# Kernel optimization log

Measured on AMD Instinct MI355X. Metric: run time of the kernel, lower is better.

Reference implementation:

```python
import jax, jax.numpy as jnp
import numpy as np

THRESHOLD = 0.9
EPS = 1e-12


def setup_inputs() -> dict:
    key = jax.random.key(0)
    ks = jax.random.split(key, 7)
    B, D_in, H1, H2, D_out = 8192, 256, 512, 256, 64
    # torch Linear default init ~ U(-1/sqrt(fan_in), 1/sqrt(fan_in)); randn scaled is fine as a stand-in
    def lin(k, out_f, in_f):
        return jax.random.normal(k, (out_f, in_f), dtype=jnp.float32) / np.sqrt(in_f)
    return {
        "x": jax.random.normal(ks[0], (B, D_in), dtype=jnp.float32),
        "W1": lin(ks[1], H1, D_in),
        "b1": jax.random.normal(ks[2], (H1,), dtype=jnp.float32) * 0.01,
        "W2": lin(ks[3], H2, H1),
        "b2": jax.random.normal(ks[4], (H2,), dtype=jnp.float32) * 0.01,
        "W3": lin(ks[5], D_out, H2),
        "b3": jax.random.normal(ks[6], (D_out,), dtype=jnp.float32) * 0.01,
    }


def reference(x, W1, b1, W2, b2, W3, b3):
    # MLP: Linear -> Tanh -> Linear -> Tanh -> Linear (no tanh on last)
    h1 = jnp.tanh(x @ W1.T + b1)          # [B, 512]
    h2 = jnp.tanh(h1 @ W2.T + b2)         # [B, 256]
    out = h2 @ W3.T + b3                  # [B, 64]

    # Pairwise state fidelity: (normalized dot)^2, thresholded adjacency (diag excluded)
    norms = jnp.linalg.norm(out, axis=-1, keepdims=True)  # [B, 1]
    normed = out / (norms + EPS)
    fid = (normed @ normed.T) ** 2                         # [B, B]
    adj = (fid >= THRESHOLD).astype(out.dtype)
    B = out.shape[0]
    adj = adj * (1.0 - jnp.eye(B, dtype=out.dtype))        # no self-edges (i < j pairs only)

    return adj @ out                                       # [B, 64]
```

## Files before the change

kernel.cpp:

```cpp
#include <hip/hip_runtime.h>
#include <hip/hip_bf16.h>
#include <math.h>

#define B_ROWS 8192
#define D_IN   256
#define H1_DIM 512
#define H2_DIM 256
#define D_OUT  64
#define EPSF   1e-12f
#define THRESH 0.9f
#define BAND_LO 0.89f
#define BAND_HI 0.91f

typedef __attribute__((ext_vector_type(8))) short short8;
typedef __attribute__((ext_vector_type(4))) float f32x4;

__device__ inline void pack8(const float* __restrict__ src, short* __restrict__ dh,
                             short* __restrict__ dm, int t, int C, int lgq) {
  const int lane = t & 63;
  const int g = t >> 6;
  const int q = g & ((1 << lgq) - 1);
  const int I = g >> lgq;
  const int row = I * 16 + (lane & 15);
  const int k0 = q * 32 + ((lane >> 4) << 3);
  const float* p = src + (size_t)row * C + k0;
  float4 a = *(const float4*)p;
  float4 b = *(const float4*)(p + 4);
  float v[8] = {a.x, a.y, a.z, a.w, b.x, b.y, b.z, b.w};
  short h8[8], m8[8];
#pragma unroll
  for (int e = 0; e < 8; ++e) {
    __hip_bfloat16 h = __float2bfloat16(v[e]);
    float hf = __bfloat162float(h);
    __hip_bfloat16 m = __float2bfloat16(v[e] - hf);
    h8[e] = *(short*)&h;
    m8[e] = *(short*)&m;
  }
  *(short8*)(dh + (size_t)t * 8) = *(short8*)h8;
  *(short8*)(dm + (size_t)t * 8) = *(short8*)m8;
}

__global__ __launch_bounds__(256)
void pack_inputs(const float* __restrict__ x, const float* __restrict__ W1,
                 const float* __restrict__ W2, const float* __restrict__ W3,
                 short* xh, short* xm, short* w1h, short* w1m,
                 short* w2h, short* w2m, short* w3h, short* w3m) {
  const int b = blockIdx.x;
  const int tid = threadIdx.x;
  if (b < 1024)       pack8(x,  xh,  xm,  b * 256 + tid, 256, 3);
  else if (b < 1088)  pack8(W1, w1h, w1m, (b - 1024) * 256 + tid, 256, 3);
  else if (b < 1152)  pack8(W2, w2h, w2m, (b - 1088) * 256 + tid, 512, 4);
  else                pack8(W3, w3h, w3m, (b - 1152) * 256 + tid, 256, 3);
}

template<int KSTEPS, int JT, int MODE>
__global__ __launch_bounds__(256, 2)
void mfma_gemm(const short* __restrict__ pAh, const short* __restrict__ pAm,
               const short* __restrict__ pBh, const short* __restrict__ pBm,
               const float* __restrict__ bias, float* __restrict__ Cout,
               short* __restrict__ dh, short* __restrict__ dm, int N,
               float* __restrict__ rz) {
  constexpr int ITB = 4;
  constexpr int BTJ = 2 * JT;
  constexpr int NITEMS = 2 * ITB + 2 * BTJ;
  constexpr int PER_WAVE = NITEMS / 4;
  constexpr int WCOL = 16 * JT + 4;
  union SM {
    struct {
      short Ah[2][ITB * 512];
      short Am[2][ITB * 512];
      short Bh[2][BTJ * 512];
      short Bm[2][BTJ * 512];
    } st;
    float wbuf[4 * 32 * WCOL];
  };
  __shared__ __align__(16) SM sm;
  __shared__ float nsum[2][64];
  __shared__ float invn[64];

  const int tid = threadIdx.x;
  const int wave = tid >> 6, lane = tid & 63;
  const int wi = wave >> 1, wj = wave & 1;
  const int bIt0 = blockIdx.x * ITB;
  const int bJt0 = blockIdx.y * BTJ;

  if constexpr (MODE == 2) {
    float4* rz4 = (float4*)(rz + (size_t)blockIdx.x * 64 * 64);
#pragma unroll
    for (int u = 0; u < 4; ++u)
      rz4[u * 256 + tid] = make_float4(0.f, 0.f, 0.f, 0.f);
  }

  f32x4 acc[2][JT];
#pragma unroll
  for (int a = 0; a < 2; ++a)
#pragma unroll
    for (int b = 0; b < JT; ++b) acc[a][b] = (f32x4){0.f, 0.f, 0.f, 0.f};

  auto stage = [&](int q, int bf) {
#pragma unroll
    for (int u = 0; u < PER_WAVE; ++u) {
      const int item = wave * PER_WAVE + u;
      const short* src;
      short* dst;
      if (item < 2 * ITB) {
        const int t = item >> 1;
        const int m = item & 1;
        src = (m ? pAm : pAh) + ((size_t)(bIt0 + t) * KSTEPS + q) * 512;
        dst = (m ? sm.st.Am : sm.st.Ah)[bf] + t * 512;
      } else {
        const int e = item - 2 * ITB;
        const int t = e >> 1;
        const int m = e & 1;
        src = (m ? pBm : pBh) + ((size_t)(bJt0 + t) * KSTEPS + q) * 512;
        dst = (m ? sm.st.Bm : sm.st.Bh)[bf] + t * 512;
      }
      __builtin_amdgcn_global_load_lds(
          (const __attribute__((address_space(1))) void*)(src + lane * 8),
          (__attribute__((address_space(3))) void*)dst, 16, 0, 0);
    }
  };

  stage(0, 0);
  for (int q = 0; q < KSTEPS; ++q) {
    __syncthreads();
    if (q + 1 < KSTEPS) stage(q + 1, (q + 1) & 1);
    const int bf = q & 1;
    short8 Ah[2], Am[2];
#pragma unroll
    for (int it = 0; it < 2; ++it) {
      Ah[it] = *(const short8*)(sm.st.Ah[bf] + (wi * 2 + it) * 512 + lane * 8);
      Am[it] = *(const short8*)(sm.st.Am[bf] + (wi * 2 + it) * 512 + lane * 8);
    }
    short8 Bh[JT], Bm[JT];
#pragma unroll
    for (int jt = 0; jt < JT; ++jt) {
      Bh[jt] = *(const short8*)(sm.st.Bh[bf] + (wj * JT + jt) * 512 + lane * 8);
      Bm[jt] = *(const short8*)(sm.st.Bm[bf] + (wj * JT + jt) * 512 + lane * 8);
    }
#pragma unroll
    for (int it = 0; it < 2; ++it)
#pragma unroll
      for (int jt = 0; jt < JT; ++jt) {
        acc[it][jt] = __builtin_amdgcn_mfma_f32_16x16x32_bf16(Ah[it], Bh[jt], acc[it][jt], 0, 0, 0);
        acc[it][jt] = __builtin_amdgcn_mfma_f32_16x16x32_bf16(Ah[it], Bm[jt], acc[it][jt], 0, 0, 0);
        acc[it][jt] = __builtin_amdgcn_mfma_f32_16x16x32_bf16(Am[it], Bh[jt], acc[it][jt], 0, 0, 0);
      }
  }
  __syncthreads();

  float bv[JT];
#pragma unroll
  for (int jt = 0; jt < JT; ++jt)
    bv[jt] = bias[(bJt0 + wj * JT + jt) * 16 + (lane & 15)];

  if constexpr (MODE == 1) {
#pragma unroll
    for (int it = 0; it < 2; ++it)
#pragma unroll
      for (int jt = 0; jt < JT; ++jt)
#pragma unroll
        for (int r = 0; r < 4; ++r) {
          const float val = tanhf(acc[it][jt][r] + bv[jt]);
          const int row_l = it * 16 + (lane >> 4) * 4 + r;
          const int col_l = jt * 16 + (lane & 15);
          sm.wbuf[(wave * 32 + row_l) * WCOL + col_l] = val;
        }
    __syncthreads();
  } else {
#pragma unroll
    for (int it = 0; it < 2; ++it)
#pragma unroll
      for (int r = 0; r < 4; ++r) {
        float sq = 0.f;
        const int row_l = it * 16 + (lane >> 4) * 4 + r;
#pragma unroll
        for (int jt = 0; jt < JT; ++jt) {
          const float val = acc[it][jt][r] + bv[jt];
          const int col_l = jt * 16 + (lane & 15);
          sm.wbuf[(wave * 32 + row_l) * WCOL + col_l] = val;
          const int row = (bIt0 + wi * 2 + it) * 16 + (lane >> 4) * 4 + r;
          Cout[(size_t)row * N + wj * (16 * JT) + col_l] = val;
          sq = fmaf(val, val, sq);
        }
#pragma unroll
        for (int m = 1; m < 16; m <<= 1) sq += __shfl_xor(sq, m, 64);
        if ((lane & 15) == 0) nsum[wj][wi * 32 + row_l] = sq;
      }
    __syncthreads();
    if (tid < 64) invn[tid] = 1.0f / (sqrtf(nsum[0][tid] + nsum[1][tid]) + EPSF);
    __syncthreads();
  }

  constexpr int QLMAX = (JT >= 2) ? (JT / 2) : 1;
#pragma unroll
  for (int itl = 0; itl < 2; ++itl)
#pragma unroll
    for (int ql = 0; ql < QLMAX; ++ql) {
      const int row_l = itl * 16 + (lane & 15);
      const int kl = ql * 32 + ((lane >> 4) << 3);
      const float* wp = &sm.wbuf[(wave * 32 + row_l) * WCOL + kl];
      const float scale = (MODE == 2) ? invn[wi * 32 + row_l] : 1.0f;
      float4 a = *(const float4*)wp;
      float4 b = *(const float4*)(wp + 4);
      float v[8] = {a.x, a.y, a.z, a.w, b.x, b.y, b.z, b.w};
      short h8[8], m8[8];
#pragma unroll
      for (int e = 0; e < 8; ++e) {
        const float sv = v[e] * scale;
        __hip_bfloat16 h = __float2bfloat16(sv);
        float hf = __bfloat162float(h);
        __hip_bfloat16 m = __float2bfloat16(sv - hf);
        h8[e] = *(short*)&h;
        m8[e] = *(short*)&m;
      }
      const int ItG = bIt0 + wi * 2 + itl;
      const int qG = (((bJt0 + wj * JT) * 16) + ql * 32) >> 5;
      const size_t off = ((size_t)(ItG * (N >> 5) + qG) * 64 + lane) * 8;
      *(short8*)(dh + off) = *(short8*)h8;
      *(short8*)(dm + off) = *(short8*)m8;
    }
}

__global__ __launch_bounds__(256, 2)
void gram_accum(const short* __restrict__ vph, const short* __restrict__ vpm,
                const float* __restrict__ out, float* __restrict__ res) {
  __shared__ __align__(16) short lAh[8 * 1024];
  __shared__ __align__(16) short lAm[8 * 1024];
  const int tid = threadIdx.x;
  const int wave = tid >> 6, lane = tid & 63;

  const int t = blockIdx.x;
  int I = (int)((129.0f - sqrtf(16641.0f - 8.0f * (float)t)) * 0.5f);
  if (I < 0) I = 0;
  while (64 * (I + 1) - ((I + 1) * I) / 2 <= t) ++I;
  while (64 * I - (I * (I - 1)) / 2 > t) --I;
  const int Jc = I + (t - (64 * I - (I * (I - 1)) / 2));
  const int i0 = I * 128;
  const int j0c = Jc * 128;

  {
    const size_t base = (size_t)I * 8192;
#pragma unroll
    for (int u = 0; u < 8; ++u) {
      const int item = wave * 8 + u;
      const short* src;
      short* dst;
      if (item < 16) { src = vph + base + item * 512; dst = lAh + item * 512; }
      else           { src = vpm + base + (item - 16) * 512; dst = lAm + (item - 16) * 512; }
      __builtin_amdgcn_global_load_lds(
          (const __attribute__((address_space(1))) void*)(src + lane * 8),
          (__attribute__((address_space(3))) void*)dst, 16, 0, 0);
    }
  }
  __syncthreads();

  short8 Ah[8][2];
#pragma unroll
  for (int it = 0; it < 8; ++it)
#pragma unroll
    for (int q = 0; q < 2; ++q)
      Ah[it][q] = *(const short8*)(lAh + it * 1024 + q * 512 + lane * 8);

#pragma unroll
  for (int tt = 0; tt < 2; ++tt) {
    const int jt = wave * 2 + tt;
    const int j0 = j0c + jt * 16;
    const short* jb_h = vph + (size_t)(j0 >> 4) * 1024;
    short8 Bh0 = *(const short8*)(jb_h + lane * 8);
    short8 Bh1 = *(const short8*)(jb_h + 512 + lane * 8);

    f32x4 g[8];
#pragma unroll
    for (int it = 0; it < 8; ++it) g[it] = (f32x4){0.f, 0.f, 0.f, 0.f};
#pragma unroll
    for (int it = 0; it < 8; ++it) g[it] = __builtin_amdgcn_mfma_f32_16x16x32_bf16(Ah[it][0], Bh0, g[it], 0, 0, 0);
#pragma unroll
    for (int it = 0; it < 8; ++it) g[it] = __builtin_amdgcn_mfma_f32_16x16x32_bf16(Ah[it][1], Bh1, g[it], 0, 0, 0);

    bool band = false;
#pragma unroll
    for (int it = 0; it < 8; ++it)
#pragma unroll
      for (int r = 0; r < 4; ++r) {
        const float f = g[it][r] * g[it][r];
        band = band || (f > BAND_LO && f < BAND_HI);
      }
    if (__any(band)) {
      const short* jb_m = vpm + (size_t)(j0 >> 4) * 1024;
      short8 Bm0 = *(const short8*)(jb_m + lane * 8);
      short8 Bm1 = *(const short8*)(jb_m + 512 + lane * 8);
#pragma unroll
      for (int it = 0; it < 8; ++it) g[it] = __builtin_amdgcn_mfma_f32_16x16x32_bf16(Ah[it][0], Bm0, g[it], 0, 0, 0);
#pragma unroll
      for (int it = 0; it < 8; ++it) g[it] = __builtin_amdgcn_mfma_f32_16x16x32_bf16(Ah[it][1], Bm1, g[it], 0, 0, 0);
#pragma unroll
      for (int it = 0; it < 8; ++it) {
        short8 Am0 = *(const short8*)(lAm + it * 1024 + lane * 8);
        short8 Am1 = *(const short8*)(lAm + it * 1024 + 512 + lane * 8);
        g[it] = __builtin_amdgcn_mfma_f32_16x16x32_bf16(Am0, Bh0, g[it], 0, 0, 0);
        g[it] = __builtin_amdgcn_mfma_f32_16x16x32_bf16(Am1, Bh1, g[it], 0, 0, 0);
      }
    }

    const int j = j0 + (lane & 15);
#pragma unroll
    for (int it = 0; it < 8; ++it) {
      const float m01 = fmaxf(g[it][0] * g[it][0], g[it][1] * g[it][1]);
      const float m23 = fmaxf(g[it][2] * g[it][2], g[it][3] * g[it][3]);
      if (fmaxf(m01, m23) >= THRESH) {
        const float* __restrict__ oj = out + (size_t)j * D_OUT;
#pragma unroll
        for (int r = 0; r < 4; ++r) {
          if (g[it][r] * g[it][r] >= THRESH) {
            const int i = i0 + it * 16 + (lane >> 4) * 4 + r;
            if (i < j) {
              float* __restrict__ ri = res + (size_t)i * D_OUT;
              float* __restrict__ rj = res + (size_t)j * D_OUT;
              const float* __restrict__ oi = out + (size_t)i * D_OUT;
              for (int k = 0; k < D_OUT; ++k) {
                atomicAdd(&ri[k], oj[k]);
                atomicAdd(&rj[k], oi[k]);
              }
            }
          }
        }
      }
    }
  }
}

#define MB (1024 * 1024)

extern "C" void kernel_launch(void* const* d_in, const int* in_sizes, int n_in,
                              void* d_out, int out_size, void* d_ws, size_t ws_size,
                              hipStream_t stream) {
  const float* x  = (const float*)d_in[0];
  const float* W1 = (const float*)d_in[1];
  const float* b1 = (const float*)d_in[2];
  const float* W2 = (const float*)d_in[3];
  const float* b2 = (const float*)d_in[4];
  const float* W3 = (const float*)d_in[5];
  const float* b3 = (const float*)d_in[6];
  float* res = (float*)d_out;

  char* ws = (char*)d_ws;
  short* xh  = (short*)(ws + 0 * MB);
  short* xm  = (short*)(ws + 4 * MB);
  short* h2h = (short*)(ws + 0 * MB);
  short* h2m = (short*)(ws + 4 * MB);
  short* h1h = (short*)(ws + 8 * MB);
  short* h1m = (short*)(ws + 16 * MB);
  float* out = (float*)(ws + 8 * MB);
  short* vph = (short*)(ws + 11 * MB);
  short* vpm = (short*)(ws + 12 * MB);
  short* w1h = (short*)(ws + 24 * MB);
  short* w1m = (short*)(ws + 24 * MB + 256 * 1024);
  short* w2h = (short*)(ws + 24 * MB + 512 * 1024);
  short* w2m = (short*)(ws + 24 * MB + 768 * 1024);
  short* w3h = (short*)(ws + 25 * MB);
  short* w3m = (short*)(ws + 25 * MB + 32 * 1024);

  pack_inputs<<<1160, 256, 0, stream>>>(x, W1, W2, W3, xh, xm, w1h, w1m, w2h, w2m, w3h, w3m);
  mfma_gemm<8, 4, 1><<<dim3(128, 4), 256, 0, stream>>>(
      xh, xm, w1h, w1m, b1, nullptr, h1h, h1m, H1_DIM, nullptr);
  mfma_gemm<16, 2, 1><<<dim3(128, 4), 256, 0, stream>>>(
      h1h, h1m, w2h, w2m, b2, nullptr, h2h, h2m, H2_DIM, nullptr);
  mfma_gemm<8, 2, 2><<<dim3(128, 1), 256, 0, stream>>>(
      h2h, h2m, w3h, w3m, b3, out, vph, vpm, D_OUT, res);
  gram_accum<<<dim3(2080), 256, 0, stream>>>(vph, vpm, out, res);
}
```

Baseline: 128.1 us.

## Fuse input packing and three MLP layers into one per-row-block kernel

Replaces the pack kernel and three separate GEMM launches with a single fused_mlp kernel. Each block handles 32 rows, keeps h1 and h2 in LDS as bf16 hi/lo splits, and reads the weights directly from global memory, splitting them on the fly. This removes the global round-trips for the intermediate activations and four launches. It also swaps tanhf for an exp-based fast tanh. The costs are only 256 blocks, large LDS use, redundant weight splitting in every block, and no double-buffered staging.

```diff
diff --git a/kernel.cpp b/kernel.cpp
--- a/kernel.cpp
+++ b/kernel.cpp
@@ -15,211 +15,270 @@
 typedef __attribute__((ext_vector_type(8))) short short8;
 typedef __attribute__((ext_vector_type(4))) float f32x4;
 
-__device__ inline void pack8(const float* __restrict__ src, short* __restrict__ dh,
-                             short* __restrict__ dm, int t, int C, int lgq) {
-  const int lane = t & 63;
-  const int g = t >> 6;
-  const int q = g & ((1 << lgq) - 1);
-  const int I = g >> lgq;
-  const int row = I * 16 + (lane & 15);
-  const int k0 = q * 32 + ((lane >> 4) << 3);
-  const float* p = src + (size_t)row * C + k0;
-  float4 a = *(const float4*)p;
-  float4 b = *(const float4*)(p + 4);
+__device__ inline float tanh_fast(float xx) {
+  const float ax = fabsf(xx);
+  const float t = __expf(-2.0f * ax);
+  const float r = (1.0f - t) / (1.0f + t);
+  return xx < 0.0f ? -r : r;
+}
+
+__device__ inline void splitf8(float4 a, float4 b, short8& h, short8& m) {
   float v[8] = {a.x, a.y, a.z, a.w, b.x, b.y, b.z, b.w};
   short h8[8], m8[8];
 #pragma unroll
   for (int e = 0; e < 8; ++e) {
-    __hip_bfloat16 h = __float2bfloat16(v[e]);
-    float hf = __bfloat162float(h);
-    __hip_bfloat16 m = __float2bfloat16(v[e] - hf);
-    h8[e] = *(short*)&h;
-    m8[e] = *(short*)&m;
-  }
-  *(short8*)(dh + (size_t)t * 8) = *(short8*)h8;
-  *(short8*)(dm + (size_t)t * 8) = *(short8*)m8;
+    __hip_bfloat16 hb = __float2bfloat16(v[e]);
+    float hf = __bfloat162float(hb);
+    __hip_bfloat16 mb = __float2bfloat16(v[e] - hf);
+    h8[e] = *(short*)&hb;
+    m8[e] = *(short*)&mb;
+  }
+  h = *(short8*)h8;
+  m = *(short8*)m8;
 }
 
-__global__ __launch_bounds__(256)
-void pack_inputs(const float* __restrict__ x, const float* __restrict__ W1,
-                 const float* __restrict__ W2, const float* __restrict__ W3,
-                 short* xh, short* xm, short* w1h, short* w1m,
-                 short* w2h, short* w2m, short* w3h, short* w3m) {
-  const int b = blockIdx.x;
-  const int tid = threadIdx.x;
-  if (b < 1024)       pack8(x,  xh,  xm,  b * 256 + tid, 256, 3);
-  else if (b < 1088)  pack8(W1, w1h, w1m, (b - 1024) * 256 + tid, 256, 3);
-  else if (b < 1152)  pack8(W2, w2h, w2m, (b - 1088) * 256 + tid, 512, 4);
-  else                pack8(W3, w3h, w3m, (b - 1152) * 256 + tid, 256, 3);
-}
-
-template<int KSTEPS, int JT, int MODE>
-__global__ __launch_bounds__(256, 2)
-void mfma_gemm(const short* __restrict__ pAh, const short* __restrict__ pAm,
-               const short* __restrict__ pBh, const short* __restrict__ pBm,
-               const float* __restrict__ bias, float* __restrict__ Cout,
-               short* __restrict__ dh, short* __restrict__ dm, int N,
-               float* __restrict__ rz) {
-  constexpr int ITB = 4;
-  constexpr int BTJ = 2 * JT;
-  constexpr int NITEMS = 2 * ITB + 2 * BTJ;
-  constexpr int PER_WAVE = NITEMS / 4;
-  constexpr int WCOL = 16 * JT + 4;
-  union SM {
-    struct {
-      short Ah[2][ITB * 512];
-      short Am[2][ITB * 512];
-      short Bh[2][BTJ * 512];
-      short Bm[2][BTJ * 512];
-    } st;
-    float wbuf[4 * 32 * WCOL];
-  };
-  __shared__ __align__(16) SM sm;
-  __shared__ float nsum[2][64];
-  __shared__ float invn[64];
+__global__ __launch_bounds__(512, 2)
+void fused_mlp(const float* __restrict__ x,  const float* __restrict__ W1,
+               const float* __restrict__ b1, const float* __restrict__ W2,
+               const float* __restrict__ b2, const float* __restrict__ W3,
+               const float* __restrict__ b3, float* __restrict__ out,
+               short* __restrict__ vph, short* __restrict__ vpm,
+               float* __restrict__ res) {
+  constexpr int WC = 260;
+  __shared__ __align__(16) union {
+    struct { short h[8192]; short m[8192]; } xp;
+    struct { short h[8192]; short m[8192]; } h2p;
+  } uAB;
+  __shared__ __align__(16) short h1h[16384];
+  __shared__ __align__(16) short h1m[16384];
+  __shared__ __align__(16) float wbuf[32 * WC];
+  __shared__ float nsum[32];
+  __shared__ float invn[32];
 
   const int tid = threadIdx.x;
   const int wave = tid >> 6, lane = tid & 63;
-  const int wi = wave >> 1, wj = wave & 1;
-  const int bIt0 = blockIdx.x * ITB;
-  const int bJt0 = blockIdx.y * BTJ;
-
-  if constexpr (MODE == 2) {
-    float4* rz4 = (float4*)(rz + (size_t)blockIdx.x * 64 * 64);
-#pragma unroll
-    for (int u = 0; u < 4; ++u)
-      rz4[u * 256 + tid] = make_float4(0.f, 0.f, 0.f, 0.f);
-  }
-
-  f32x4 acc[2][JT];
-#pragma unroll
-  for (int a = 0; a < 2; ++a)
-#pragma unroll
-    for (int b = 0; b < JT; ++b) acc[a][b] = (f32x4){0.f, 0.f, 0.f, 0.f};
-
-  auto stage = [&](int q, int bf) {
-#pragma unroll
-    for (int u = 0; u < PER_WAVE; ++u) {
-      const int item = wave * PER_WAVE + u;
-      const short* src;
-      short* dst;
-      if (item < 2 * ITB) {
-        const int t = item >> 1;
-        const int m = item & 1;
-        src = (m ? pAm : pAh) + ((size_t)(bIt0 + t) * KSTEPS + q) * 512;
-        dst = (m ? sm.st.Am : sm.st.Ah)[bf] + t * 512;
-      } else {
-        const int e = item - 2 * ITB;
-        const int t = e >> 1;
-        const int m = e & 1;
-        src = (m ? pBm : pBh) + ((size_t)(bJt0 + t) * KSTEPS + q) * 512;
-        dst = (m ? sm.st.Bm : sm.st.Bh)[bf] + t * 512;
-      }
-      __builtin_amdgcn_global_load_lds(
-          (const __attribute__((address_space(1))) void*)(src + lane * 8),
-          (__attribute__((address_space(3))) void*)dst, 16, 0, 0);
-    }
-  };
-
-  stage(0, 0);
-  for (int q = 0; q < KSTEPS; ++q) {
+  const int r0 = blockIdx.x * 32;
+  const int col16 = lane & 15;
+  const int k8 = (lane >> 4) << 3;
+  const int rbase = (lane >> 4) * 2 * 2;
+
+  {
+    float4* rz = (float4*)(res + (size_t)r0 * D_OUT);
+    rz[tid] = make_float4(0.f, 0.f, 0.f, 0.f);
+  }
+
+#pragma unroll
+  for (int uu = 0; uu < 2; ++uu) {
+    const int u = tid + uu * 512;
+    const int lu = u & 63, g = u >> 6;
+    const int q = g & 7, I = g >> 3;
+    const float* p = x + (size_t)(r0 + I * 16 + (lu & 15)) * D_IN + q * 32 + ((lu >> 4) << 3);
+    float4 a = *(const float4*)p, b = *(const float4*)(p + 4);
+    short8 hh, mm;
+    splitf8(a, b, hh, mm);
+    const int off = ((I * 8 + q) * 64 + lu) * 8;
+    *(short8*)(uAB.xp.h + off) = hh;
+    *(short8*)(uAB.xp.m + off) = mm;
+  }
+  __syncthreads();
+
+  f32x4 acc1[2][4];
+#pragma unroll
+  for (int it = 0; it < 2; ++it)
+#pragma unroll
+    for (int jj = 0; jj < 4; ++jj) acc1[it][jj] = (f32x4){0.f, 0.f, 0.f, 0.f};
+
+#pragma unroll 4
+  for (int q = 0; q < 8; ++q) {
+    short8 Ah[2], Am[2];
+#pragma unroll
+    for (int it = 0; it < 2; ++it) {
+      const int off = ((it * 8 + q) * 64 + lane) * 8;
+      Ah[it] = *(const short8*)(uAB.xp.h + off);
+      Am[it] = *(const short8*)(uAB.xp.m + off);
+    }
+    short8 Bh[4], Bm[4];
+#pragma unroll
+    for (int jj = 0; jj < 4; ++jj) {
+      const float* wp = W1 + (size_t)((wave * 4 + jj) * 16 + col16) * D_IN + q * 32 + k8;
+      splitf8(*(const float4*)wp, *(const float4*)(wp + 4), Bh[jj], Bm[jj]);
+    }
+#pragma unroll
+    for (int it = 0; it < 2; ++it)
+#pragma unroll
+      for (int jj = 0; jj < 4; ++jj) {
+        acc1[it][jj] = __builtin_amdgcn_mfma_f32_16x16x32_bf16(Ah[it], Bh[jj], acc1[it][jj], 0, 0, 0);
+        acc1[it][jj] = __builtin_amdgcn_mfma_f32_16x16x32_bf16(Ah[it], Bm[jj], acc1[it][jj], 0, 0, 0);
+        acc1[it][jj] = __builtin_amdgcn_mfma_f32_16x16x32_bf16(Am[it], Bh[jj], acc1[it][jj], 0, 0, 0);
+      }
+  }
+
+  float bv1[4];
+#pragma unroll
+  for (int jj = 0; jj < 4; ++jj) bv1[jj] = b1[(wave * 4 + jj) * 16 + col16];
+
+#pragma unroll
+  for (int h = 0; h < 2; ++h) {
+    if ((wave >> 2) == h) {
+#pragma unroll
+      for (int it = 0; it < 2; ++it)
+#pragma unroll
+        for (int jj = 0; jj < 4; ++jj)
+#pragma unroll
+          for (int r = 0; r < 4; ++r) {
+            const int row = it * 16 + rbase + r;
+            const int col = ((wave & 3) * 4 + jj) * 16 + col16;
+            wbuf[row * WC + col] = tanh_fast(acc1[it][jj][r] + bv1[jj]);
+          }
+    }
     __syncthreads();
-    if (q + 1 < KSTEPS) stage(q + 1, (q + 1) & 1);
-    const int bf = q & 1;
+#pragma unroll
+    for (int uu = 0; uu < 2; ++uu) {
+      const int u = tid + uu * 512;
+      const int lu = u & 63, g = u >> 6;
+      const int ql = g & 7, it = g >> 3;
+      const int row = it * 16 + (lu & 15);
+      const int kl = ql * 32 + ((lu >> 4) << 3);
+      const float* wp = &wbuf[row * WC + kl];
+      short8 hh, mm;
+      splitf8(*(const float4*)wp, *(const float4*)(wp + 4), hh, mm);
+      const int off = ((it * 16 + h * 8 + ql) * 64 + lu) * 8;
+      *(short8*)(h1h + off) = hh;
+      *(short8*)(h1m + off) = mm;
+    }
+    __syncthreads();
+  }
+
+  f32x4 acc2[2][2];
+#pragma unroll
+  for (int it = 0; it < 2; ++it)
+#pragma unroll
+    for (int jj = 0; jj < 2; ++jj) acc2[it][jj] = (f32x4){0.f, 0.f, 0.f, 0.f};
+
+#pragma unroll 4
+  for (int q = 0; q < 16; ++q) {
     short8 Ah[2], Am[2];
 #pragma unroll
     for (int it = 0; it < 2; ++it) {
-      Ah[it] = *(const short8*)(sm.st.Ah[bf] + (wi * 2 + it) * 512 + lane * 8);
-      Am[it] = *(const short8*)(sm.st.Am[bf] + (wi * 2 + it) * 512 + lane * 8);
-    }
-    short8 Bh[JT], Bm[JT];
-#pragma unroll
-    for (int jt = 0; jt < JT; ++jt) {
-      Bh[jt] = *(const short8*)(sm.st.Bh[bf] + (wj * JT + jt) * 512 + lane * 8);
-      Bm[jt] = *(const short8*)(sm.st.Bm[bf] + (wj * JT + jt) * 512 + lane * 8);
+      const int off = ((it * 16 + q) * 64 + lane) * 8;
+      Ah[it] = *(const short8*)(h1h + off);
+      Am[it] = *(const short8*)(h1m + off);
+    }
+    short8 Bh[2], Bm[2];
+#pragma unroll
+    for (int jj = 0; jj < 2; ++jj) {
+      const float* wp = W2 + (size_t)((wave * 2 + jj) * 16 + col16) * H1_DIM + q * 32 + k8;
+      splitf8(*(const float4*)wp, *(const float4*)(wp + 4), Bh[jj], Bm[jj]);
     }
 #pragma unroll
     for (int it = 0; it < 2; ++it)
 #pragma unroll
-      for (int jt = 0; jt < JT; ++jt) {
-        acc[it][jt] = __builtin_amdgcn_mfma_f32_16x16x32_bf16(Ah[it], Bh[jt], acc[it][jt], 0, 0, 0);
-        acc[it][jt] = __builtin_amdgcn_mfma_f32_16x16x32_bf16(Ah[it], Bm[jt], acc[it][jt], 0, 0, 0);
-        acc[it][jt] = __builtin_amdgcn_mfma_f32_16x16x32_bf16(Am[it], Bh[jt], acc[it][jt], 0, 0, 0);
-      }
-  }
-  __syncthreads();
-
-  float bv[JT];
-#pragma unroll
-  for (int jt = 0; jt < JT; ++jt)
-    bv[jt] = bias[(bJt0 + wj * JT + jt) * 16 + (lane & 15)];
-
-  if constexpr (MODE == 1) {
+      for (int jj = 0; jj < 2; ++jj) {
+        acc2[it][jj] = __builtin_amdgcn_mfma_f32_16x16x32_bf16(Ah[it], Bh[jj], acc2[it][jj], 0, 0, 0);
+        acc2[it][jj] = __builtin_amdgcn_mfma_f32_16x16x32_bf16(Ah[it], Bm[jj], acc2[it][jj], 0, 0, 0);
+        acc2[it][jj] = __builtin_amdgcn_mfma_f32_16x16x32_bf16(Am[it], Bh[jj], acc2[it][jj], 0, 0, 0);
+      }
+  }
+
+  {
+    float bv2[2];
+#pragma unroll
+    for (int jj = 0; jj < 2; ++jj) bv2[jj] = b2[(wave * 2 + jj) * 16 + col16];
 #pragma unroll
     for (int it = 0; it < 2; ++it)
 #pragma unroll
-      for (int jt = 0; jt < JT; ++jt)
+      for (int jj = 0; jj < 2; ++jj)
 #pragma unroll
         for (int r = 0; r < 4; ++r) {
-          const float val = tanhf(acc[it][jt][r] + bv[jt]);
-          const int row_l = it * 16 + (lane >> 4) * 4 + r;
-          const int col_l = jt * 16 + (lane & 15);
-          sm.wbuf[(wave * 32 + row_l) * WCOL + col_l] = val;
+          const int row = it * 16 + rbase + r;
+          const int col = (wave * 2 + jj) * 16 + col16;
+          wbuf[row * WC + col] = tanh_fast(acc2[it][jj][r] + bv2[jj]);
         }
-    __syncthreads();
-  } else {
+  }
+  __syncthreads();
+#pragma unroll
+  for (int uu = 0; uu < 2; ++uu) {
+    const int u = tid + uu * 512;
+    const int lu = u & 63, g = u >> 6;
+    const int ql = g & 7, it = g >> 3;
+    const int row = it * 16 + (lu & 15);
+    const int kl = ql * 32 + ((lu >> 4) << 3);
+    const float* wp = &wbuf[row * WC + kl];
+    short8 hh, mm;
+    splitf8(*(const float4*)wp, *(const float4*)(wp + 4), hh, mm);
+    const int off = ((it * 8 + ql) * 64 + lu) * 8;
+    *(short8*)(uAB.h2p.h + off) = hh;
+    *(short8*)(uAB.h2p.m + off) = mm;
+  }
+  __syncthreads();
+
+  if (wave < 4) {
+    f32x4 acc3[2];
+#pragma unroll
+    for (int it = 0; it < 2; ++it) acc3[it] = (f32x4){0.f, 0.f, 0.f, 0.f};
+#pragma unroll
+    for (int q = 0; q < 8; ++q) {
+      short8 Ah[2], Am[2];
+#pragma unroll
+      for (int it = 0; it < 2; ++it) {
+        const int off = ((it * 8 + q) * 64 + lane) * 8;
+        Ah[it] = *(const short8*)(uAB.h2p.h + off);
+        Am[it] = *(const short8*)(uAB.h2p.m + off);
+      }
+      short8 Bh, Bm;
+      const float* wp = W3 + (size_t)(wave * 16 + col16) * H2_DIM + q * 32 + k8;
+      splitf8(*(const float4*)wp, *(const float4*)(wp + 4), Bh, Bm);
+#pragma unroll
+      for (int it = 0; it < 2; ++it) {
+        acc3[it] = __builtin_amdgcn_mfma_f32_16x16x32_bf16(Ah[it], Bh, acc3[it], 0, 0, 0);
+        acc3[it] = __builtin_amdgcn_mfma_f32_16x16x32_bf16(Ah[it], Bm, acc3[it], 0, 0, 0);
+        acc3[it] = __builtin_amdgcn_mfma_f32_16x16x32_bf16(Am[it], Bh, acc3[it], 0, 0, 0);
+      }
+    }
+    const float bv3 = b3[wave * 16 + col16];
 #pragma unroll
     for (int it = 0; it < 2; ++it)
 #pragma unroll
-      for (int r = 0; r < 4; ++r) {
-        float sq = 0.f;
-        const int row_l = it * 16 + (lane >> 4) * 4 + r;
-#pragma unroll
-        for (int jt = 0; jt < JT; ++jt) {
-          const float val = acc[it][jt][r] + bv[jt];
-          const int col_l = jt * 16 + (lane & 15);
-          sm.wbuf[(wave * 32 + row_l) * WCOL + col_l] = val;
-          const int row = (bIt0 + wi * 2 + it) * 16 + (lane >> 4) * 4 + r;
-          Cout[(size_t)row * N + wj * (16 * JT) + col_l] = val;
-          sq = fmaf(val, val, sq);
-        }
-#pragma unroll
-        for (int m = 1; m < 16; m <<= 1) sq += __shfl_xor(sq, m, 64);
-        if ((lane & 15) == 0) nsum[wj][wi * 32 + row_l] = sq;
-      }
-    __syncthreads();
-    if (tid < 64) invn[tid] = 1.0f / (sqrtf(nsum[0][tid] + nsum[1][tid]) + EPSF);
-    __syncthreads();
-  }
-
-  constexpr int QLMAX = (JT >= 2) ? (JT / 2) : 1;
-#pragma unroll
-  for (int itl = 0; itl < 2; ++itl)
-#pragma unroll
-    for (int ql = 0; ql < QLMAX; ++ql) {
-      const int row_l = itl * 16 + (lane & 15);
-      const int kl = ql * 32 + ((lane >> 4) << 3);
-      const float* wp = &sm.wbuf[(wave * 32 + row_l) * WCOL + kl];
-      const float scale = (MODE == 2) ? invn[wi * 32 + row_l] : 1.0f;
-      float4 a = *(const float4*)wp;
-      float4 b = *(const float4*)(wp + 4);
-      float v[8] = {a.x, a.y, a.z, a.w, b.x, b.y, b.z, b.w};
-      short h8[8], m8[8];
-#pragma unroll
-      for (int e = 0; e < 8; ++e) {
-        const float sv = v[e] * scale;
-        __hip_bfloat16 h = __float2bfloat16(sv);
-        float hf = __bfloat162float(h);
-        __hip_bfloat16 m = __float2bfloat16(sv - hf);
-        h8[e] = *(short*)&h;
-        m8[e] = *(short*)&m;
-      }
-      const int ItG = bIt0 + wi * 2 + itl;
-      const int qG = (((bJt0 + wj * JT) * 16) + ql * 32) >> 5;
-      const size_t off = ((size_t)(ItG * (N >> 5) + qG) * 64 + lane) * 8;
-      *(short8*)(dh + off) = *(short8*)h8;
-      *(short8*)(dm + off) = *(short8*)m8;
-    }
+      for (int r = 0; r < 4; ++r)
+        wbuf[(it * 16 + rbase + r) * WC + wave * 16 + col16] = acc3[it][r] + bv3;
+  }
+  __syncthreads();
+
+  if (tid < 256) {
+    const int row = tid >> 3, c0 = (tid & 7) * 8;
+    const float* wp = &wbuf[row * WC + c0];
+    float4 a = *(const float4*)wp, b = *(const float4*)(wp + 4);
+    float s = a.x * a.x + a.y * a.y + a.z * a.z + a.w * a.w +
+              b.x * b.x + b.y * b.y + b.z * b.z + b.w * b.w;
+    s += __shfl_xor(s, 1, 64);
+    s += __shfl_xor(s, 2, 64);
+    s += __shfl_xor(s, 4, 64);
+    if ((tid & 7) == 0) nsum[row] = s;
+  }
+  __syncthreads();
+  if (tid < 32) invn[tid] = 1.0f / (sqrtf(nsum[tid]) + EPSF);
+  __syncthreads();
+
+  {
+    const int row = tid >> 4, c4 = (tid & 15) * 4;
+    *(float4*)(out + (size_t)(r0 + row) * D_OUT + c4) = *(const float4*)&wbuf[row * WC + c4];
+  }
+  if (tid < 256) {
+    const int lu = tid & 63, g = tid >> 6;
+    const int ql = g & 1, it = g >> 1;
+    const int row = it * 16 + (lu & 15);
+    const int kl = ql * 32 + ((lu >> 4) << 3);
+    const float sc = invn[row];
+    const float* wp = &wbuf[row * WC + kl];
+    float4 a = *(const float4*)wp, b = *(const float4*)(wp + 4);
+    a.x *= sc; a.y *= sc; a.z *= sc; a.w *= sc;
+    b.x *= sc; b.y *= sc; b.z *= sc; b.w *= sc;
+    short8 hh, mm;
+    splitf8(a, b, hh, mm);
+    const size_t off = (((size_t)(blockIdx.x * 2 + it) * 2 + ql) * 64 + lu) * 8;
+    *(short8*)(vph + off) = hh;
+    *(short8*)(vpm + off) = mm;
+  }
 }
 
 __global__ __launch_bounds__(256, 2)
@@ -345,28 +404,10 @@
   float* res = (float*)d_out;
 
   char* ws = (char*)d_ws;
-  short* xh  = (short*)(ws + 0 * MB);
-  short* xm  = (short*)(ws + 4 * MB);
-  short* h2h = (short*)(ws + 0 * MB);
-  short* h2m = (short*)(ws + 4 * MB);
-  short* h1h = (short*)(ws + 8 * MB);
-  short* h1m = (short*)(ws + 16 * MB);
-  float* out = (float*)(ws + 8 * MB);
-  short* vph = (short*)(ws + 11 * MB);
-  short* vpm = (short*)(ws + 12 * MB);
-  short* w1h = (short*)(ws + 24 * MB);
-  short* w1m = (short*)(ws + 24 * MB + 256 * 1024);
-  short* w2h = (short*)(ws + 24 * MB + 512 * 1024);
-  short* w2m = (short*)(ws + 24 * MB + 768 * 1024);
-  short* w3h = (short*)(ws + 25 * MB);
-  short* w3m = (short*)(ws + 25 * MB + 32 * 1024);
-
-  pack_inputs<<<1160, 256, 0, stream>>>(x, W1, W2, W3, xh, xm, w1h, w1m, w2h, w2m, w3h, w3m);
-  mfma_gemm<8, 4, 1><<<dim3(128, 4), 256, 0, stream>>>(
-      xh, xm, w1h, w1m, b1, nullptr, h1h, h1m, H1_DIM, nullptr);
-  mfma_gemm<16, 2, 1><<<dim3(128, 4), 256, 0, stream>>>(
-      h1h, h1m, w2h, w2m, b2, nullptr, h2h, h2m, H2_DIM, nullptr);
-  mfma_gemm<8, 2, 2><<<dim3(128, 1), 256, 0, stream>>>(
-      h2h, h2m, w3h, w3m, b3, out, vph, vpm, D_OUT, res);
+  float* out = (float*)(ws);
+  short* vph = (short*)(ws + 2 * MB);
+  short* vpm = (short*)(ws + 3 * MB);
+
+  fused_mlp<<<256, 512, 0, stream>>>(x, W1, b1, W2, b2, W3, b3, out, vph, vpm, res);
   gram_accum<<<dim3(2080), 256, 0, stream>>>(vph, vpm, out, res);
 }
```

New measurement: 129.1 us. Within noise of the previous version (+0.8%).
